# Kernel optimization log

Measured on AMD Instinct MI355X. Metric: run time of the kernel, lower is better.

Reference implementation:

```python
import jax, jax.numpy as jnp
import numpy as np

LOG2E = 1.4426950408889634
NUM_HEADS = 12

def fake_quant_sym8(x):
    # per-tensor symmetric int8 fake-quant (QuantStub with MovingAverageMinMax,
    # symmetric, qint8 [-128,127]); dynamic scale from current amax, STE.
    scale = jnp.maximum(jnp.max(jnp.abs(x)) / 127.0, 1e-8)
    q = jnp.clip(jnp.round(x / scale), -128.0, 127.0) * scale
    return x + jax.lax.stop_gradient(q - x)

def integer_approx_softmax(x):
    # ITA-style integer-approximated softmax: exp(x) = 2^(x*log2e),
    # split into integer/fractional parts, 2^f approximated piecewise-linearly
    # as (1 + f) for f in [0,1) (hardware shift-add friendly), then normalize.
    z = x * LOG2E
    z = z - jnp.max(z, axis=-1, keepdims=True)  # z <= 0, numerically stable
    zi = jnp.floor(z)
    zf = z - zi
    p = jnp.exp2(zi) * (1.0 + zf)
    return p / jnp.sum(p, axis=-1, keepdims=True)

def setup_inputs() -> dict:
    key = jax.random.key(0)
    ks = jax.random.split(key, 5)
    B, N, E, P = 8, 1024, 768, 768
    s = 0.02  # typical init scale for linear weights
    return {
        "x":  jax.random.normal(ks[0], (B, N, E), jnp.float32),
        "Wq": jax.random.normal(ks[1], (E, P), jnp.float32) * s,
        "bq": jnp.zeros((P,), jnp.float32),
        "Wk": jax.random.normal(ks[2], (E, P), jnp.float32) * s,
        "bk": jnp.zeros((P,), jnp.float32),
        "Wv": jax.random.normal(ks[3], (E, P), jnp.float32) * s,
        "bv": jnp.zeros((P,), jnp.float32),
        "Wo": jax.random.normal(ks[4], (P, E), jnp.float32) * s,
        "bo": jnp.zeros((E,), jnp.float32),
    }

def reference(x, Wq, bq, Wk, bk, Wv, bv, Wo, bo):
    B, N, E = x.shape
    H = NUM_HEADS
    D = Wq.shape[1] // H  # head_dim = proj_dim // num_heads
    xq = fake_quant_sym8(x)
    # projections -> [B, H, N, D]
    Q = (xq @ Wq + bq).reshape(B, N, H, D).transpose(0, 2, 1, 3)
    K = (xq @ Wk + bk).reshape(B, N, H, D).transpose(0, 2, 1, 3)
    V = (xq @ Wv + bv).reshape(B, N, H, D).transpose(0, 2, 1, 3)
    # NOTE: no 1/sqrt(D) scaling -- the torch module applies none (ITA absorbs
    # scaling into the quantization parameters).
    logits = jnp.einsum('bhnd,bhmd->bhnm', Q, K)
    attn = integer_approx_softmax(logits)
    ctx = jnp.einsum('bhnm,bhmd->bhnd', attn, V)
    ctx = ctx.transpose(0, 2, 1, 3).reshape(B, N, H * D)
    return ctx @ Wo + bo
```

## Files before the change

### kernel.cpp

```cpp
#include <hip/hip_runtime.h>


typedef unsigned short u16;
typedef __attribute__((ext_vector_type(8))) short short8;
typedef __attribute__((ext_vector_type(8))) _Float16 half8;
typedef __attribute__((ext_vector_type(4))) float f32x4;

#define LOG2E_F 1.4426950408889634f

static __device__ __forceinline__ half8 s2h(short8 s) {
  union { short8 s; half8 h; } u; u.s = s; return u.h;
}
static __device__ __forceinline__ f32x4 mfma16(short8 a, short8 b, f32x4 c) {
  return __builtin_amdgcn_mfma_f32_16x16x32_f16(s2h(a), s2h(b), c, 0, 0, 0);
}
static __device__ __forceinline__ u16 f2h(float f) {
  union { _Float16 h; u16 u; } v; v.h = (_Float16)f; return v.u;
}
static __device__ __forceinline__ float ita_p(float zz) {
  zz = fmaxf(zz, -126.0f);
  float t = fmaf(zz, 8388608.0f, 1065353216.0f);
  union { int i; float f; } c;
  c.i = (int)t;
  return c.f;
}
static __device__ __forceinline__ void gload16(const void* g, void* l) {
  __builtin_amdgcn_global_load_lds(
      (const __attribute__((address_space(1))) void*)g,
      (__attribute__((address_space(3))) void*)l, 16, 0, 0);
}

__global__ __launch_bounds__(256) void amax_part_kernel(
    const float4* __restrict__ x, float* __restrict__ part, int n4) {
  float m = 0.f;
  int i = blockIdx.x * 256 + threadIdx.x;
  const int stride = gridDim.x * 256;
  for (; i < n4; i += stride) {
    float4 v = x[i];
    m = fmaxf(m, fmaxf(fmaxf(fabsf(v.x), fabsf(v.y)),
                       fmaxf(fabsf(v.z), fabsf(v.w))));
  }
  #pragma unroll
  for (int o = 1; o < 64; o <<= 1) m = fmaxf(m, __shfl_xor(m, o));
  __shared__ float sw[4];
  if ((threadIdx.x & 63) == 0) sw[threadIdx.x >> 6] = m;
  __syncthreads();
  if (threadIdx.x == 0)
    part[blockIdx.x] = fmaxf(fmaxf(sw[0], sw[1]), fmaxf(sw[2], sw[3]));
}

__global__ __launch_bounds__(256) void amax_fin_kernel(
    const float* __restrict__ part, double* __restrict__ dsc,
    float* __restrict__ dscf) {
  const int t = threadIdx.x;
  float m = fmaxf(fmaxf(part[t], part[t + 256]),
                  fmaxf(part[t + 512], part[t + 768]));
  #pragma unroll
  for (int o = 1; o < 64; o <<= 1) m = fmaxf(m, __shfl_xor(m, o));
  __shared__ float sw[4];
  if ((t & 63) == 0) sw[t >> 6] = m;
  __syncthreads();
  if (t == 0) {
    double sd = (double)(fmaxf(fmaxf(sw[0], sw[1]), fmaxf(sw[2], sw[3]))) / 127.0;
    if (sd < 1e-8) sd = 1e-8;
    dsc[0] = sd;
    dsc[1] = 1.0 / sd;
    dscf[0] = (float)sd;
  }
}

__global__ __launch_bounds__(256) void quant_kernel(
    const float4* __restrict__ x, u16* __restrict__ xq,
    const double* __restrict__ dsc, int n4) {
  const double rinv = dsc[1];
  int i = blockIdx.x * 256 + threadIdx.x;
  const int stride = gridDim.x * 256;
  for (; i < n4; i += stride) {
    float4 v = x[i];
    ushort4 u;
    u.x = f2h((float)fmin(fmax(rint((double)v.x * rinv), -128.0), 127.0));
    u.y = f2h((float)fmin(fmax(rint((double)v.y * rinv), -128.0), 127.0));
    u.z = f2h((float)fmin(fmax(rint((double)v.z * rinv), -128.0), 127.0));
    u.w = f2h((float)fmin(fmax(rint((double)v.w * rinv), -128.0), 127.0));
    *(ushort4*)&xq[(size_t)i * 4] = u;
  }
}

__global__ __launch_bounds__(256) void prep_weights_kernel(
    const float* __restrict__ Wq, const float* __restrict__ Wk,
    const float* __restrict__ Wv, const float* __restrict__ Wo,
    const float* __restrict__ bq, const float* __restrict__ bk,
    const float* __restrict__ bv,
    u16* __restrict__ Wcat, u16* __restrict__ Wot, float* __restrict__ bcat) {
  __shared__ float t[64][65];
  const int m = blockIdx.y;
  const float* src = (m == 0) ? Wq : (m == 1) ? Wk : (m == 2) ? Wv : Wo;
  u16* dst = (m == 3) ? Wot : (Wcat + (size_t)m * 768 * 768);
  const int tile = blockIdx.x;
  const int r0 = (tile / 12) * 64, c0 = (tile - (tile / 12) * 12) * 64;
  const int i = threadIdx.x >> 6, j = threadIdx.x & 63;
  #pragma unroll
  for (int it = 0; it < 16; ++it) {
    const int row = it * 4 + i;
    t[row][j] = src[(size_t)(r0 + row) * 768 + c0 + j];
  }
  __syncthreads();
  #pragma unroll
  for (int it = 0; it < 16; ++it) {
    const int row = it * 4 + i;
    dst[(size_t)(c0 + row) * 768 + r0 + j] = f2h(t[j][row]);
  }
  if (blockIdx.x == 0 && m == 0) {
    for (int k = threadIdx.x; k < 768; k += 256) {
      bcat[k] = bq[k];
      bcat[k + 768] = bk[k];
      bcat[k + 1536] = bv[k];
    }
  }
}

template <int MODE>
__global__ __launch_bounds__(256, 4) void gemm128(
    const u16* __restrict__ A, const u16* __restrict__ Bt,
    const float* __restrict__ bias, const float* __restrict__ scale_p,
    u16* __restrict__ Oq, u16* __restrict__ Ok, u16* __restrict__ Ovt,
    float* __restrict__ Of) {
  __shared__ u16 S[4][4608];
  const int K = 768, nk = 24;
  const int tid = threadIdx.x;
  const int w = tid >> 6, l = tid & 63;
  const int l15 = l & 15, lk = l >> 4;
  const int wr = w >> 1, wc = w & 1;
  const int bid = blockIdx.x;
  const int g = bid & 7, li = bid >> 3;
  const int tn = li >> 3, tm = g * 8 + (li & 7);
  f32x4 acc[4][4] = {};
  const int rA = tid >> 2;
  const int c8 = (((tid & 3) ^ ((tid >> 3) & 3))) * 8;
  const int xs = (l15 >> 1) & 3;
  const u16* gA = A + (size_t)(tm * 128 + rA) * K + c8;
  const u16* gB = Bt + (size_t)(tn * 128 + rA) * K + c8;
  {
    char* lA = (char*)S[0] + w * 1024;
    char* lB = (char*)S[2] + w * 1024;
    gload16(gA, lA);
    gload16(gA + (size_t)64 * K, lA + 4096);
    gload16(gB, lB);
    gload16(gB + (size_t)64 * K, lB + 4096);
  }
  __syncthreads();
  for (int kt = 0; kt < nk; ++kt) {
    const int buf = kt & 1;
    if (kt + 1 < nk) {
      const int k0 = (kt + 1) * 32;
      char* lA = (char*)S[buf ^ 1] + w * 1024;
      char* lB = (char*)S[2 + (buf ^ 1)] + w * 1024;
      gload16(gA + k0, lA);
      gload16(gA + k0 + (size_t)64 * K, lA + 4096);
      gload16(gB + k0, lB);
      gload16(gB + k0 + (size_t)64 * K, lB + 4096);
    }
    short8 af[4], bf[4];
    #pragma unroll
    for (int mi = 0; mi < 4; ++mi)
      af[mi] = *(const short8*)
          &S[buf][(wr * 64 + mi * 16 + l15) * 32 + (lk ^ xs) * 8];
    #pragma unroll
    for (int ni = 0; ni < 4; ++ni)
      bf[ni] = *(const short8*)
          &S[2 + buf][(wc * 64 + ni * 16 + l15) * 32 + (lk ^ xs) * 8];
    #pragma unroll
    for (int mi = 0; mi < 4; ++mi)
      #pragma unroll
      for (int ni = 0; ni < 4; ++ni)
        acc[mi][ni] = mfma16(af[mi], bf[ni], acc[mi][ni]);
    __syncthreads();
  }

  if (MODE == 1) {
    #pragma unroll
    for (int mi = 0; mi < 4; ++mi)
      #pragma unroll
      for (int ni = 0; ni < 4; ++ni)
        #pragma unroll
        for (int j = 0; j < 4; ++j) {
          const int gm = tm * 128 + wr * 64 + mi * 16 + lk * 4 + j;
          const int c = tn * 128 + wc * 64 + ni * 16 + l15;
          Of[(size_t)gm * 768 + c] = acc[mi][ni][j] + bias[c];
        }
    return;
  }

  __syncthreads();
  const float s = *scale_p;
  const int seg = tn / 6;
  const int h = (tn - seg * 6) * 2 + wc;
  u16* esc = &S[w][0];
  #pragma unroll
  for (int mi = 0; mi < 4; ++mi) {
    #pragma unroll
    for (int ni = 0; ni < 4; ++ni) {
      #pragma unroll
      for (int j = 0; j < 4; ++j) {
        const float v = acc[mi][ni][j] * s + bias[tn * 128 + wc * 64 + ni * 16 + l15];
        const int row = mi * 16 + lk * 4 + j;
        const int col = ni * 16 + l15;
        if (seg < 2) esc[row * 72 + col] = f2h(v);
        else         esc[col * 72 + row] = f2h(v);
      }
    }
  }
  asm volatile("s_waitcnt lgkmcnt(0)" ::: "memory");
  const int n0 = tm * 128 + wr * 64;
  const int b = n0 >> 10, nn = n0 & 1023;
  u16* outp = (seg == 0) ? Oq : (seg == 1) ? Ok : Ovt;
  #pragma unroll
  for (int it = 0; it < 8; ++it) {
    const int r = it * 8 + (l >> 3);
    const int cc = (l & 7) * 8;
    short8 vv = *(const short8*)&esc[r * 72 + cc];
    size_t o;
    if (seg < 2)
      o = (((size_t)b * 12 + h) * 1024 + nn + r) * 64 + cc;
    else
      o = (((size_t)b * 12 + h) * 64 + r) * 1024 + nn + cc;
    *(short8*)&outp[o] = vv;
  }
}

__global__ __launch_bounds__(256, 3) void attn_kernel(
    const u16* __restrict__ Q, const u16* __restrict__ K,
    const u16* __restrict__ Vt, u16* __restrict__ ctx) {
  __shared__ u16 lds[4 * 4096 + 4 * 1280];
  u16* const ldsK = lds;
  u16* const ldsV = lds + 8192;
  const int bh = blockIdx.x, qt = blockIdx.y;
  const int b = bh / 12, h = bh - b * 12;
  const int tid = threadIdx.x;
  const int w = tid >> 6, l = tid & 63;
  const int l15 = l & 15, lk = l >> 4;
  const int xr = l15 & 7;

  short8 qa[2][2];
  #pragma unroll
  for (int rf = 0; rf < 2; ++rf) {
    const size_t qoff =
        ((size_t)bh * 1024 + qt * 128 + w * 32 + rf * 16 + l15) * 64 + lk * 8;
    qa[rf][0] = *(const short8*)(Q + qoff);
    qa[rf][1] = *(const short8*)(Q + qoff + 32);
  }

  const int r8 = l >> 3;
  const int schunk = ((l & 7) ^ r8) * 8;
  const u16* Kg0 = K + ((size_t)bh * 1024 + w * 16 + r8) * 64 + schunk;
  const u16* Kg1 = Kg0 + 512;
  const u16* Vg0 = Vt + ((size_t)bh * 64 + w * 16 + r8) * 1024 + schunk;
  const u16* Vg1 = Vg0 + 8192;

  #define STAGE_KA(buf, kt)                                                 \
    {                                                                       \
      gload16(Kg0 + (size_t)(kt) * 4096, &ldsK[(buf) * 4096 + w * 1024]);   \
      gload16(Kg1 + (size_t)(kt) * 4096,                                    \
              &ldsK[(buf) * 4096 + w * 1024 + 512]);                        \
    }
  #define STAGE_V(buf, kt)                                                  \
    {                                                                       \
      gload16(Vg0 + (size_t)(kt) * 64, &ldsV[(buf) * 4096 + w * 1024]);     \
      gload16(Vg1 + (size_t)(kt) * 64,                                      \
              &ldsV[(buf) * 4096 + w * 1024 + 512]);                        \
    }

  f32x4 mx[2];
  #pragma unroll
  for (int rf = 0; rf < 2; ++rf)
    #pragma unroll
    for (int j = 0; j < 4; ++j) mx[rf][j] = -3e38f;
  STAGE_KA(0, 0)
  STAGE_KA(1, 1)
  __syncthreads();
  for (int st = 0; st < 8; ++st) {
    if (st < 7) {
      STAGE_KA((2 * st + 2) & 3, 2 * st + 2)
      STAGE_KA((2 * st + 3) & 3, 2 * st + 3)
    }
    #pragma unroll
    for (int hf = 0; hf < 2; ++hf) {
      const u16* kb = &ldsK[((2 * st + hf) & 3) * 4096];
      #pragma unroll
      for (int ks = 0; ks < 4; ++ks) {
        short8 k0 = *(const short8*)&kb[(ks * 16 + l15) * 64 + ((lk ^ xr) * 8)];
        short8 k1 = *(const short8*)&kb[(ks * 16 + l15) * 64 + (((lk + 4) ^ xr) * 8)];
        #pragma unroll
        for (int rf = 0; rf < 2; ++rf) {
          f32x4 sv = {0.f, 0.f, 0.f, 0.f};
          sv = mfma16(qa[rf][0], k0, sv);
          sv = mfma16(qa[rf][1], k1, sv);
          #pragma unroll
          for (int j = 0; j < 4; ++j) mx[rf][j] = fmaxf(mx[rf][j], sv[j]);
        }
      }
    }
    __syncthreads();
  }
  f32x4 negmz[2];
  #pragma unroll
  for (int rf = 0; rf < 2; ++rf) {
    #pragma unroll
    for (int o = 1; o < 16; o <<= 1) {
      #pragma unroll
      for (int j = 0; j < 4; ++j)
        mx[rf][j] = fmaxf(mx[rf][j], __shfl_xor(mx[rf][j], o));
    }
    #pragma unroll
    for (int j = 0; j < 4; ++j) negmz[rf][j] = -(mx[rf][j] * LOG2E_F);
  }

  f32x4 sum[2] = {};
  f32x4 pv[2][4] = {};
  u16* const pw = &lds[16384 + w * 1280];
  STAGE_KA(0, 0)
  STAGE_V(0, 0)
  __syncthreads();
  for (int kt = 0; kt < 16; ++kt) {
    const int buf = kt & 1;
    if (kt < 15) {
      STAGE_KA(buf ^ 1, kt + 1)
      STAGE_V(buf ^ 1, kt + 1)
    }
    const u16* kb = &ldsK[buf * 4096];
    const u16* vb = &ldsV[buf * 4096];
    #pragma unroll
    for (int ko = 0; ko < 2; ++ko) {
      #pragma unroll
      for (int ks2 = 0; ks2 < 2; ++ks2) {
        const int ks = ko * 2 + ks2;
        short8 k0 = *(const short8*)&kb[(ks * 16 + l15) * 64 + ((lk ^ xr) * 8)];
        short8 k1 = *(const short8*)&kb[(ks * 16 + l15) * 64 + (((lk + 4) ^ xr) * 8)];
        #pragma unroll
        for (int rf = 0; rf < 2; ++rf) {
          f32x4 sv = {0.f, 0.f, 0.f, 0.f};
          sv = mfma16(qa[rf][0], k0, sv);
          sv = mfma16(qa[rf][1], k1, sv);
          #pragma unroll
          for (int j = 0; j < 4; ++j) {
            float p = ita_p(fmaf(sv[j], LOG2E_F, negmz[rf][j]));
            sum[rf][j] += p;
            pw[(rf * 16 + lk * 4 + j) * 40 + ks2 * 16 + l15] = f2h(p);
          }
        }
      }
      asm volatile("s_waitcnt lgkmcnt(0)" ::: "memory");
      short8 pa0 = *(const short8*)&pw[l15 * 40 + lk * 8];
      short8 pa1 = *(const short8*)&pw[(16 + l15) * 40 + lk * 8];
      #pragma unroll
      for (int dt = 0; dt < 4; ++dt) {
        short8 vv = *(const short8*)&vb[(dt * 16 + l15) * 64 +
                                        (((lk + 4 * ko) ^ xr) * 8)];
        pv[0][dt] = mfma16(pa0, vv, pv[0][dt]);
        pv[1][dt] = mfma16(pa1, vv, pv[1][dt]);
      }
    }
    __syncthreads();
  }
  #undef STAGE_KA
  #undef STAGE_V
  #pragma unroll
  for (int rf = 0; rf < 2; ++rf) {
    #pragma unroll
    for (int o = 1; o < 16; o <<= 1) {
      #pragma unroll
      for (int j = 0; j < 4; ++j) sum[rf][j] += __shfl_xor(sum[rf][j], o);
    }
    const int nrow = qt * 128 + w * 32 + rf * 16 + lk * 4;
    #pragma unroll
    for (int dt = 0; dt < 4; ++dt) {
      #pragma unroll
      for (int j = 0; j < 4; ++j) {
        float v = pv[rf][dt][j] / sum[rf][j];
        ctx[((size_t)b * 1024 + nrow + j) * 768 + h * 64 + dt * 16 + l15] =
            f2h(v);
      }
    }
  }
}

extern "C" void kernel_launch(void* const* d_in, const int* in_sizes, int n_in,
                              void* d_out, int out_size, void* d_ws, size_t ws_size,
                              hipStream_t stream) {
  const float* x  = (const float*)d_in[0];
  const float* Wq = (const float*)d_in[1];
  const float* bq = (const float*)d_in[2];
  const float* Wk = (const float*)d_in[3];
  const float* bk = (const float*)d_in[4];
  const float* Wv = (const float*)d_in[5];
  const float* bv = (const float*)d_in[6];
  const float* Wo = (const float*)d_in[7];
  const float* bo = (const float*)d_in[8];
  float* out = (float*)d_out;

  char* ws = (char*)d_ws;
  float* part  = (float*)ws;
  double* dsc  = (double*)(ws + 4096);
  float* dscf  = (float*)(ws + 4112);
  float* bcat  = (float*)(ws + 8192);
  size_t off = 8192 + 16384;
  const size_t WB = (size_t)768 * 768;
  const size_t XB = (size_t)8192 * 768;
  u16* xq   = (u16*)(ws + off); off += XB * 2;
  u16* Wcat = (u16*)(ws + off); off += 3 * WB * 2;
  u16* Wot  = (u16*)(ws + off); off += WB * 2;
  u16* Qb   = (u16*)(ws + off); off += XB * 2;
  u16* Kb   = (u16*)(ws + off); off += XB * 2;
  u16* Vtb  = (u16*)(ws + off); off += XB * 2;
  u16* ctx  = xq;
  (void)ws_size; (void)in_sizes; (void)n_in; (void)out_size;

  const int n4 = (8 * 1024 * 768) / 4;
  amax_part_kernel<<<1024, 256, 0, stream>>>((const float4*)x, part, n4);
  amax_fin_kernel<<<1, 256, 0, stream>>>(part, dsc, dscf);
  quant_kernel<<<2048, 256, 0, stream>>>((const float4*)x, xq, dsc, n4);
  prep_weights_kernel<<<dim3(144, 4), 256, 0, stream>>>(
      Wq, Wk, Wv, Wo, bq, bk, bv, Wcat, Wot, bcat);
  gemm128<0><<<1152, 256, 0, stream>>>(xq, Wcat, bcat, dscf,
                                       Qb, Kb, Vtb, nullptr);
  attn_kernel<<<dim3(96, 8), 256, 0, stream>>>(Qb, Kb, Vtb, ctx);
  gemm128<1><<<384, 256, 0, stream>>>(ctx, Wot, bo, nullptr,
                                      nullptr, nullptr, nullptr, out);
}
```

Before: 149.5 us.

## Enlarge GEMM tile to 256x128 per block for QKV and output projections

Doubles the M dimension of each GEMM block tile from 128 to 256, so each wave computes a 128x64 sub-tile with 8x4 accumulators and reuses each B fragment across eight A fragments. Block-to-tile mapping changes to group along N, and the QKV epilogue now writes two 64-row halves through the LDS staging buffer in sequence. This halves the grid sizes and cuts B-tile global/LDS traffic per flop. In exchange it uses more registers and LDS per block, lowers occupancy to 3, and gives fewer blocks (192 for the output projection) on a large-CU GPU.

```diff
diff --git a/kernel.cpp b/kernel.cpp
--- a/kernel.cpp
+++ b/kernel.cpp
@@ -120,71 +120,73 @@
 }
 
 template <int MODE>
-__global__ __launch_bounds__(256, 4) void gemm128(
+__global__ __launch_bounds__(256, 3) void gemm256(
     const u16* __restrict__ A, const u16* __restrict__ Bt,
     const float* __restrict__ bias, const float* __restrict__ scale_p,
     u16* __restrict__ Oq, u16* __restrict__ Ok, u16* __restrict__ Ovt,
     float* __restrict__ Of) {
-  __shared__ u16 S[4][4608];
+  __shared__ u16 S[2 * 8192 + 2 * 4096];
+  u16* const AsB = S;
+  u16* const BsB = S + 16384;
   const int K = 768, nk = 24;
   const int tid = threadIdx.x;
   const int w = tid >> 6, l = tid & 63;
   const int l15 = l & 15, lk = l >> 4;
   const int wr = w >> 1, wc = w & 1;
+  const int NT = (MODE == 0) ? 18 : 6;
   const int bid = blockIdx.x;
   const int g = bid & 7, li = bid >> 3;
-  const int tn = li >> 3, tm = g * 8 + (li & 7);
-  f32x4 acc[4][4] = {};
+  const int tm = g * 4 + li / NT;
+  const int tn = li % NT;
+  f32x4 acc[8][4] = {};
   const int rA = tid >> 2;
   const int c8 = (((tid & 3) ^ ((tid >> 3) & 3))) * 8;
   const int xs = (l15 >> 1) & 3;
-  const u16* gA = A + (size_t)(tm * 128 + rA) * K + c8;
+  const u16* gA = A + (size_t)(tm * 256 + rA) * K + c8;
   const u16* gB = Bt + (size_t)(tn * 128 + rA) * K + c8;
-  {
-    char* lA = (char*)S[0] + w * 1024;
-    char* lB = (char*)S[2] + w * 1024;
-    gload16(gA, lA);
-    gload16(gA + (size_t)64 * K, lA + 4096);
-    gload16(gB, lB);
-    gload16(gB + (size_t)64 * K, lB + 4096);
-  }
+
+  #define STG(buf, k0)                                                  \
+    {                                                                   \
+      char* lA = (char*)(AsB + (buf) * 8192) + w * 1024;                \
+      char* lB = (char*)(BsB + (buf) * 4096) + w * 1024;                \
+      gload16(gA + (k0), lA);                                           \
+      gload16(gA + (k0) + (size_t)64 * K, lA + 4096);                   \
+      gload16(gA + (k0) + (size_t)128 * K, lA + 8192);                  \
+      gload16(gA + (k0) + (size_t)192 * K, lA + 12288);                 \
+      gload16(gB + (k0), lB);                                           \
+      gload16(gB + (k0) + (size_t)64 * K, lB + 4096);                   \
+    }
+
+  STG(0, 0)
   __syncthreads();
   for (int kt = 0; kt < nk; ++kt) {
     const int buf = kt & 1;
-    if (kt + 1 < nk) {
-      const int k0 = (kt + 1) * 32;
-      char* lA = (char*)S[buf ^ 1] + w * 1024;
-      char* lB = (char*)S[2 + (buf ^ 1)] + w * 1024;
-      gload16(gA + k0, lA);
-      gload16(gA + k0 + (size_t)64 * K, lA + 4096);
-      gload16(gB + k0, lB);
-      gload16(gB + k0 + (size_t)64 * K, lB + 4096);
-    }
-    short8 af[4], bf[4];
-    #pragma unroll
-    for (int mi = 0; mi < 4; ++mi)
-      af[mi] = *(const short8*)
-          &S[buf][(wr * 64 + mi * 16 + l15) * 32 + (lk ^ xs) * 8];
+    if (kt + 1 < nk) STG(buf ^ 1, (kt + 1) * 32)
+    const u16* as = AsB + buf * 8192;
+    const u16* bs = BsB + buf * 4096;
+    short8 bf[4];
     #pragma unroll
     for (int ni = 0; ni < 4; ++ni)
-      bf[ni] = *(const short8*)
-          &S[2 + buf][(wc * 64 + ni * 16 + l15) * 32 + (lk ^ xs) * 8];
-    #pragma unroll
-    for (int mi = 0; mi < 4; ++mi)
+      bf[ni] = *(const short8*)&bs[(wc * 64 + ni * 16 + l15) * 32 + (lk ^ xs) * 8];
+    #pragma unroll
+    for (int mi = 0; mi < 8; ++mi) {
+      short8 af = *(const short8*)&as[(wr * 128 + mi * 16 + l15) * 32 + (lk ^ xs) * 8];
       #pragma unroll
       for (int ni = 0; ni < 4; ++ni)
-        acc[mi][ni] = mfma16(af[mi], bf[ni], acc[mi][ni]);
+        acc[mi][ni] = mfma16(af, bf[ni], acc[mi][ni]);
+    }
     __syncthreads();
   }
+  #undef STG
 
   if (MODE == 1) {
     #pragma unroll
-    for (int mi = 0; mi < 4; ++mi)
+    for (int mi = 0; mi < 8; ++mi)
       #pragma unroll
       for (int ni = 0; ni < 4; ++ni)
         #pragma unroll
         for (int j = 0; j < 4; ++j) {
-          const int gm = tm * 128 + wr * 64 + mi * 16 + lk * 4 + j;
+          const int gm = tm * 256 + wr * 128 + mi * 16 + lk * 4 + j;
           const int c = tn * 128 + wc * 64 + ni * 16 + l15;
           Of[(size_t)gm * 768 + c] = acc[mi][ni][j] + bias[c];
         }
@@ -195,36 +197,42 @@
   const float s = *scale_p;
   const int seg = tn / 6;
   const int h = (tn - seg * 6) * 2 + wc;
-  u16* esc = &S[w][0];
-  #pragma unroll
-  for (int mi = 0; mi < 4; ++mi) {
-    #pragma unroll
-    for (int ni = 0; ni < 4; ++ni) {
-      #pragma unroll
-      for (int j = 0; j < 4; ++j) {
-        const float v = acc[mi][ni][j] * s + bias[tn * 128 + wc * 64 + ni * 16 + l15];
-        const int row = mi * 16 + lk * 4 + j;
-        const int col = ni * 16 + l15;
-        if (seg < 2) esc[row * 72 + col] = f2h(v);
-        else         esc[col * 72 + row] = f2h(v);
-      }
-    }
-  }
-  asm volatile("s_waitcnt lgkmcnt(0)" ::: "memory");
-  const int n0 = tm * 128 + wr * 64;
+  u16* esc = S + w * 4608;
+  const int n0 = tm * 256 + wr * 128;
   const int b = n0 >> 10, nn = n0 & 1023;
   u16* outp = (seg == 0) ? Oq : (seg == 1) ? Ok : Ovt;
   #pragma unroll
-  for (int it = 0; it < 8; ++it) {
-    const int r = it * 8 + (l >> 3);
-    const int cc = (l & 7) * 8;
-    short8 vv = *(const short8*)&esc[r * 72 + cc];
-    size_t o;
-    if (seg < 2)
-      o = (((size_t)b * 12 + h) * 1024 + nn + r) * 64 + cc;
-    else
-      o = (((size_t)b * 12 + h) * 64 + r) * 1024 + nn + cc;
-    *(short8*)&outp[o] = vv;
+  for (int hp = 0; hp < 2; ++hp) {
+    #pragma unroll
+    for (int mi2 = 0; mi2 < 4; ++mi2) {
+      const int mi = hp * 4 + mi2;
+      #pragma unroll
+      for (int ni = 0; ni < 4; ++ni) {
+        #pragma unroll
+        for (int j = 0; j < 4; ++j) {
+          const float v =
+              acc[mi][ni][j] * s + bias[tn * 128 + wc * 64 + ni * 16 + l15];
+          const int row = mi2 * 16 + lk * 4 + j;
+          const int col = ni * 16 + l15;
+          if (seg < 2) esc[row * 72 + col] = f2h(v);
+          else         esc[col * 72 + row] = f2h(v);
+        }
+      }
+    }
+    asm volatile("s_waitcnt lgkmcnt(0)" ::: "memory");
+    #pragma unroll
+    for (int it = 0; it < 8; ++it) {
+      const int r = it * 8 + (l >> 3);
+      const int cc = (l & 7) * 8;
+      short8 vv = *(const short8*)&esc[r * 72 + cc];
+      size_t o;
+      if (seg < 2)
+        o = (((size_t)b * 12 + h) * 1024 + nn + hp * 64 + r) * 64 + cc;
+      else
+        o = (((size_t)b * 12 + h) * 64 + r) * 1024 + nn + hp * 64 + cc;
+      *(short8*)&outp[o] = vv;
+    }
+    asm volatile("s_waitcnt lgkmcnt(0)" ::: "memory");
   }
 }
 
@@ -421,9 +429,9 @@
   quant_kernel<<<2048, 256, 0, stream>>>((const float4*)x, xq, dsc, n4);
   prep_weights_kernel<<<dim3(144, 4), 256, 0, stream>>>(
       Wq, Wk, Wv, Wo, bq, bk, bv, Wcat, Wot, bcat);
-  gemm128<0><<<1152, 256, 0, stream>>>(xq, Wcat, bcat, dscf,
-                                       Qb, Kb, Vtb, nullptr);
+  gemm256<0><<<576, 256, 0, stream>>>(xq, Wcat, bcat, dscf,
+                                      Qb, Kb, Vtb, nullptr);
   attn_kernel<<<dim3(96, 8), 256, 0, stream>>>(Qb, Kb, Vtb, ctx);
-  gemm128<1><<<384, 256, 0, stream>>>(ctx, Wot, bo, nullptr,
+  gemm256<1><<<192, 256, 0, stream>>>(ctx, Wot, bo, nullptr,
                                       nullptr, nullptr, nullptr, out);
 }
```

New measurement: 149.9 us, median of 2. No clear change (+0.2%).
